# Kernel optimization log

Hardware: AMD Instinct MI355X
Metric: run time of the kernel (lower is better)

The kernel has to match this reference:

```python
import jax, jax.numpy as jnp
import numpy as np

N = 100000      # nodes
E = 1000000     # edges (before self-loops)
IN_DIM = 256
H = 4           # heads
C = 32          # out_dim per head
NEG_SLOPE = 0.2  # PyG GATConv default negative_slope


def setup_inputs() -> dict:
    key = jax.random.key(0)
    ks = jax.random.split(key, 6)
    x = jax.random.normal(ks[0], (N, IN_DIM), jnp.float32)
    W = jax.random.normal(ks[1], (IN_DIM, H * C), jnp.float32) * (1.0 / np.sqrt(IN_DIM))
    a_src = jax.random.normal(ks[2], (H, C), jnp.float32) * 0.1
    a_dst = jax.random.normal(ks[3], (H, C), jnp.float32) * 0.1
    bias = jnp.zeros((H * C,), jnp.float32)
    edge_index = jax.random.randint(ks[4], (2, E), 0, N, dtype=jnp.int32)
    return {"x": x, "W": W, "a_src": a_src, "a_dst": a_dst, "bias": bias,
            "edge_index": edge_index}


def reference(x, W, a_src, a_dst, bias, edge_index):
    n = x.shape[0]
    # PyG GATConv default: add self-loops
    loops = jnp.arange(n, dtype=edge_index.dtype)
    src = jnp.concatenate([edge_index[0], loops])  # [E+N]
    dst = jnp.concatenate([edge_index[1], loops])  # [E+N]
    # linear transform -> [N, H, C]
    h = (x @ W).reshape(n, H, C)
    # per-node attention logits
    alpha_s = jnp.einsum('nhc,hc->nh', h, a_src)  # [N, H]
    alpha_d = jnp.einsum('nhc,hc->nh', h, a_dst)  # [N, H]
    # per-edge score, LeakyReLU
    e = jax.nn.leaky_relu(alpha_s[src] + alpha_d[dst], NEG_SLOPE)  # [E+N, H]
    # segment softmax over incoming edges of each destination node
    m = jax.lax.stop_gradient(jax.ops.segment_max(e, dst, num_segments=n))
    p = jnp.exp(e - m[dst])
    s = jax.ops.segment_sum(p, dst, num_segments=n)
    alpha = p / (s[dst] + 1e-16)  # [E+N, H]
    # weighted scatter-add of source features
    out = jax.ops.segment_sum(alpha[:, :, None] * h[src], dst, num_segments=n)  # [N, H, C]
    out = out.reshape(n, H * C) + bias
    return jnp.tanh(out)
```

## Files before the change

### kernel.cpp

```cpp
#include <hip/hip_runtime.h>

#define IN_DIM 256
#define HC     128
#define NHEAD  4
#define NEG    0.2f
#define BKT    1024
#define NBMAX  128
#define EPT    16
#define BE     4096

typedef __attribute__((ext_vector_type(8))) short short8v;
typedef __attribute__((ext_vector_type(4))) float f32x4;
typedef __attribute__((ext_vector_type(4))) unsigned short ushort4v;

__device__ __forceinline__ unsigned short bf16_rn(float f) {
    unsigned u = __builtin_bit_cast(unsigned, f);
    return (unsigned short)((u + 0x7fffu + ((u >> 16) & 1u)) >> 16);
}
__device__ __forceinline__ float bf16_to_f32(unsigned short b) {
    unsigned u = ((unsigned)b) << 16;
    return __builtin_bit_cast(float, u);
}
__device__ __forceinline__ float bf16_lo(unsigned v) {
    return __builtin_bit_cast(float, v << 16);
}
__device__ __forceinline__ float bf16_hi(unsigned v) {
    return __builtin_bit_cast(float, v & 0xffff0000u);
}
__device__ __forceinline__ float fast_tanh(float x) {
    float t = __expf(2.f * x);
    return fmaf(-2.f, __builtin_amdgcn_rcpf(t + 1.f), 1.f);
}
__device__ __forceinline__ float lrelu(float e) {
    return fmaxf(e, NEG * e);
}

__global__ void pack_w_kernel(const float* __restrict__ W,
                              unsigned short* __restrict__ w_hi) {
    int t = blockIdx.x * 256 + threadIdx.x;
    if (t >= 8 * 8 * 64) return;
    int l  = t & 63;
    int ct = (t >> 6) & 7;
    int s  = t >> 9;
    int kbase = s * 32 + (l >> 4) * 8;
    int col   = ct * 16 + (l & 15);
    size_t base = (size_t)t * 8;
#pragma unroll
    for (int e = 0; e < 8; ++e)
        w_hi[base + e] = bf16_rn(W[(size_t)(kbase + e) * HC + col]);
}

__global__ __launch_bounds__(512) void gemm_mfma_kernel(const float* __restrict__ x,
                                                        const unsigned short* __restrict__ w_hi,
                                                        const float* __restrict__ a_src,
                                                        const float* __restrict__ a_dst,
                                                        unsigned short* __restrict__ h_bf,
                                                        float* __restrict__ alpha_s,
                                                        float* __restrict__ alpha_d, int n) {
    __shared__ unsigned short s_bf[64 * 256];
    __shared__ float pS[64][4];
    __shared__ float pD[64][4];

    const int tid = threadIdx.x;
    const int l   = tid & 63;
    const int wv  = tid >> 6;
    const int row0 = blockIdx.x * 64;

    const float4* x4 = reinterpret_cast<const float4*>(x);
#pragma unroll
    for (int i = 0; i < 8; ++i) {
        int row = i * 8 + wv;
        int c4  = l;
        float4 v = make_float4(0.f, 0.f, 0.f, 0.f);
        if (row0 + row < n) v = x4[(size_t)(row0 + row) * 64 + c4];
        ushort4v b;
        b[0] = bf16_rn(v.x); b[1] = bf16_rn(v.y);
        b[2] = bf16_rn(v.z); b[3] = bf16_rn(v.w);
        int slot = (c4 >> 1) ^ (row & 7);
        int uidx = row * 256 + (slot << 3) + ((c4 & 1) << 2);
        *reinterpret_cast<ushort4v*>(&s_bf[uidx]) = b;
    }
    __syncthreads();

    const int ct_g = wv & 3;
    const int rt_g = wv >> 2;
    const int rrow = l & 15;
    const int kq   = l >> 4;

    f32x4 acc[2][2];
#pragma unroll
    for (int a = 0; a < 2; ++a)
#pragma unroll
        for (int b = 0; b < 2; ++b) acc[a][b] = (f32x4){0.f, 0.f, 0.f, 0.f};

    for (int s = 0; s < 8; ++s) {
        short8v bh[2];
#pragma unroll
        for (int c = 0; c < 2; ++c) {
            int ct = ct_g * 2 + c;
            bh[c] = *reinterpret_cast<const short8v*>(w_hi + ((size_t)(s * 8 + ct) * 64 + l) * 8);
        }
#pragma unroll
        for (int r = 0; r < 2; ++r) {
            int arow = rt_g * 32 + r * 16 + rrow;
            int c16  = kq + s * 4;
            int uidx = arow * 256 + ((c16 ^ (arow & 7)) << 3);
            short8v ah = *reinterpret_cast<const short8v*>(&s_bf[uidx]);
#pragma unroll
            for (int c = 0; c < 2; ++c)
                acc[r][c] = __builtin_amdgcn_mfma_f32_16x16x32_bf16(ah, bh[c], acc[r][c], 0, 0, 0);
        }
    }

#pragma unroll
    for (int r = 0; r < 2; ++r) {
#pragma unroll
        for (int c = 0; c < 2; ++c) {
            int col = (ct_g * 2 + c) * 16 + (l & 15);
#pragma unroll
            for (int q = 0; q < 4; ++q) {
                int row = row0 + rt_g * 32 + r * 16 + (l >> 4) * 4 + q;
                if (row < n) h_bf[(size_t)row * HC + col] = bf16_rn(acc[r][c][q]);
            }
        }
    }

    float asc[2], adc[2];
#pragma unroll
    for (int c = 0; c < 2; ++c) {
        int col = (ct_g * 2 + c) * 16 + (l & 15);
        asc[c] = a_src[col];
        adc[c] = a_dst[col];
    }
#pragma unroll
    for (int r = 0; r < 2; ++r) {
#pragma unroll
        for (int q = 0; q < 4; ++q) {
            float vS = acc[r][0][q] * asc[0] + acc[r][1][q] * asc[1];
            float vD = acc[r][0][q] * adc[0] + acc[r][1][q] * adc[1];
#pragma unroll
            for (int m = 1; m < 16; m <<= 1) {
                vS += __shfl_xor(vS, m);
                vD += __shfl_xor(vD, m);
            }
            if ((l & 15) == 0) {
                int rl = rt_g * 32 + r * 16 + (l >> 4) * 4 + q;
                pS[rl][ct_g] = vS;
                pD[rl][ct_g] = vD;
            }
        }
    }
    __syncthreads();
    if (tid < 256) {
        int rl = tid >> 2, h = tid & 3;
        int row = row0 + rl;
        if (row < n) {
            alpha_s[(size_t)row * 4 + h] = pS[rl][h];
            alpha_d[(size_t)row * 4 + h] = pD[rl][h];
        }
    }
}

__global__ __launch_bounds__(256) void bucket_hist_kernel(const int* __restrict__ ei,
                                                          int* __restrict__ bucket_cnt,
                                                          int E, int nb) {
    __shared__ int lh[NBMAX];
    int tid = threadIdx.x;
    if (tid < NBMAX) lh[tid] = 0;
    __syncthreads();
    int base = blockIdx.x * BE;
#pragma unroll
    for (int i = 0; i < EPT; ++i) {
        int e = base + i * 256 + tid;
        if (e < E) atomicAdd(&lh[ei[E + e] >> 10], 1);
    }
    __syncthreads();
    if (tid < nb && lh[tid]) atomicAdd(&bucket_cnt[tid], lh[tid]);
}

__global__ __launch_bounds__(128) void bucket_scan_kernel(const int* __restrict__ bucket_cnt,
                                                          int* __restrict__ bucket_base,
                                                          int* __restrict__ bucket_cursor,
                                                          int nb) {
    __shared__ int ws0[1];
    int t = threadIdx.x;
    int v = (t < nb) ? bucket_cnt[t] : 0;
    int lane = t & 63, wd = t >> 6;
    int x = v;
#pragma unroll
    for (int off = 1; off < 64; off <<= 1) {
        int y = __shfl_up(x, off);
        if (lane >= off) x += y;
    }
    if (wd == 0 && lane == 63) ws0[0] = x;
    __syncthreads();
    int wo = wd ? ws0[0] : 0;
    int excl = wo + x - v;
    if (t < nb) { bucket_base[t] = excl; bucket_cursor[t] = excl; }
    if (t == 127) bucket_base[nb] = wo + x;
}

__global__ __launch_bounds__(256) void bucket_scatter_kernel(const int* __restrict__ ei,
                                                             int* __restrict__ bucket_cursor,
                                                             unsigned* __restrict__ bucket_data,
                                                             int E, int nb) {
    __shared__ int lh[NBMAX];
    __shared__ int lofs[NBMAX];
    __shared__ int gofs[NBMAX];
    __shared__ int ws0[1];
    __shared__ unsigned buf[BE];

    int tid = threadIdx.x;
    if (tid < NBMAX) lh[tid] = 0;
    __syncthreads();

    int base = blockIdx.x * BE;
    int bb[EPT]; unsigned wv[EPT]; int rr[EPT];
#pragma unroll
    for (int i = 0; i < EPT; ++i) {
        int e = base + i * 256 + tid;
        if (e < E) {
            int src = ei[e];
            int dst = ei[E + e];
            bb[i] = dst >> 10;
            wv[i] = (unsigned)src | ((unsigned)(dst & 1023) << 17);
            rr[i] = atomicAdd(&lh[bb[i]], 1);
        } else bb[i] = -1;
    }
    __syncthreads();

    int v_ = 0, x_ = 0;
    int lane = tid & 63, wd = tid >> 6;
    if (tid < NBMAX) {
        v_ = lh[tid]; x_ = v_;
#pragma unroll
        for (int off = 1; off < 64; off <<= 1) {
            int y = __shfl_up(x_, off);
            if (lane >= off) x_ += y;
        }
        if (wd == 0 && lane == 63) ws0[0] = x_;
    }
    __syncthreads();
    if (tid < NBMAX) {
        int wo = wd ? ws0[0] : 0;
        lofs[tid] = wo + x_ - v_;
    }
    __syncthreads();

#pragma unroll
    for (int i = 0; i < EPT; ++i)
        if (bb[i] >= 0) buf[lofs[bb[i]] + rr[i]] = wv[i];
    if (tid < nb) gofs[tid] = lh[tid] ? atomicAdd(&bucket_cursor[tid], lh[tid]) : 0;
    __syncthreads();

    int wid = tid >> 6;
    for (int bk = wid; bk < nb; bk += 4) {
        int lo = lofs[bk], cnt = lh[bk], g = gofs[bk];
        for (int j = lane; j < cnt; j += 64)
            bucket_data[g + j] = buf[lo + j];
    }
}

__global__ __launch_bounds__(1024) void bucket_build_kernel(const int* __restrict__ bucket_base,
                                                            const unsigned* __restrict__ bucket_data,
                                                            int* __restrict__ deg,
                                                            int* __restrict__ row_start,
                                                            int* __restrict__ csr_src, int n) {
    __shared__ int lc[BKT];
    __shared__ int sc[BKT];
    __shared__ int wsum[16];

    int b = blockIdx.x;
    int base = bucket_base[b];
    int end  = bucket_base[b + 1];
    int t = threadIdx.x;

    lc[t] = 0;
    __syncthreads();
    for (int i = base + t; i < end; i += 1024)
        atomicAdd(&lc[bucket_data[i] >> 17], 1);
    __syncthreads();

    int val = lc[t];
    int lane = t & 63, wd = t >> 6;
    int x = val;
#pragma unroll
    for (int off = 1; off < 64; off <<= 1) {
        int y = __shfl_up(x, off);
        if (lane >= off) x += y;
    }
    if (lane == 63) wsum[wd] = x;
    __syncthreads();
    if (wd == 0 && lane < 16) {
        int y = wsum[lane];
#pragma unroll
        for (int off = 1; off < 16; off <<= 1) {
            int z = __shfl_up(y, off);
            if (lane >= off) y += z;
        }
        wsum[lane] = y;
    }
    __syncthreads();
    int wo = wd ? wsum[wd - 1] : 0;
    int excl = wo + x - val;
    sc[t] = excl;
    int v = b * BKT + t;
    if (v < n) { deg[v] = val; row_start[v] = base + excl; }
    lc[t] = 0;
    __syncthreads();

    for (int i = base + t; i < end; i += 1024) {
        unsigned w = bucket_data[i];
        int d = w >> 17;
        int src = (int)(w & 0x1FFFFu);
        int p = atomicAdd(&lc[d], 1);
        csr_src[base + sc[d] + p] = src;
    }
}

__global__ __launch_bounds__(256) void gather_kernel(const int* __restrict__ row_start,
                                                     const int* __restrict__ deg,
                                                     const int* __restrict__ csr_src,
                                                     const float* __restrict__ alpha_s,
                                                     const float* __restrict__ alpha_d,
                                                     const unsigned short* __restrict__ h_bf,
                                                     const float* __restrict__ bias,
                                                     float* __restrict__ out, int n) {
    int lane = threadIdx.x & 63;
    int wid  = threadIdx.x >> 6;
    int v = blockIdx.x * 4 + wid;
    if (v >= n) return;
    int start = row_start[v];
    int cnt = deg[v];
    int head = lane >> 4;

    const unsigned* hb = reinterpret_cast<const unsigned*>(h_bf);

    float adH = alpha_d[(size_t)v * 4 + head];
    float asH = alpha_s[(size_t)v * 4 + head];
    float pself = __expf(lrelu(asH + adH));
    unsigned hv0 = hb[((unsigned)v << 6) + lane];
    float s = pself;
    float accx = pself * bf16_lo(hv0);
    float accy = pself * bf16_hi(hv0);

    int j = 0;
    for (; j + 8 <= cnt; j += 8) {
        int s0 = csr_src[start + j + 0];
        int s1 = csr_src[start + j + 1];
        int s2 = csr_src[start + j + 2];
        int s3 = csr_src[start + j + 3];
        int s4 = csr_src[start + j + 4];
        int s5 = csr_src[start + j + 5];
        int s6 = csr_src[start + j + 6];
        int s7 = csr_src[start + j + 7];
        float a0 = alpha_s[(size_t)s0 * 4 + head];
        float a1 = alpha_s[(size_t)s1 * 4 + head];
        float a2 = alpha_s[(size_t)s2 * 4 + head];
        float a3 = alpha_s[(size_t)s3 * 4 + head];
        float a4 = alpha_s[(size_t)s4 * 4 + head];
        float a5 = alpha_s[(size_t)s5 * 4 + head];
        float a6 = alpha_s[(size_t)s6 * 4 + head];
        float a7 = alpha_s[(size_t)s7 * 4 + head];
        unsigned h0 = hb[((unsigned)s0 << 6) + lane];
        unsigned h1 = hb[((unsigned)s1 << 6) + lane];
        unsigned h2 = hb[((unsigned)s2 << 6) + lane];
        unsigned h3 = hb[((unsigned)s3 << 6) + lane];
        unsigned h4 = hb[((unsigned)s4 << 6) + lane];
        unsigned h5 = hb[((unsigned)s5 << 6) + lane];
        unsigned h6 = hb[((unsigned)s6 << 6) + lane];
        unsigned h7 = hb[((unsigned)s7 << 6) + lane];
        float w0 = __expf(lrelu(a0 + adH));
        float w1 = __expf(lrelu(a1 + adH));
        float w2 = __expf(lrelu(a2 + adH));
        float w3 = __expf(lrelu(a3 + adH));
        float w4 = __expf(lrelu(a4 + adH));
        float w5 = __expf(lrelu(a5 + adH));
        float w6 = __expf(lrelu(a6 + adH));
        float w7 = __expf(lrelu(a7 + adH));
        s += w0 + w1 + w2 + w3 + w4 + w5 + w6 + w7;
        accx = fmaf(w0, bf16_lo(h0), accx); accy = fmaf(w0, bf16_hi(h0), accy);
        accx = fmaf(w1, bf16_lo(h1), accx); accy = fmaf(w1, bf16_hi(h1), accy);
        accx = fmaf(w2, bf16_lo(h2), accx); accy = fmaf(w2, bf16_hi(h2), accy);
        accx = fmaf(w3, bf16_lo(h3), accx); accy = fmaf(w3, bf16_hi(h3), accy);
        accx = fmaf(w4, bf16_lo(h4), accx); accy = fmaf(w4, bf16_hi(h4), accy);
        accx = fmaf(w5, bf16_lo(h5), accx); accy = fmaf(w5, bf16_hi(h5), accy);
        accx = fmaf(w6, bf16_lo(h6), accx); accy = fmaf(w6, bf16_hi(h6), accy);
        accx = fmaf(w7, bf16_lo(h7), accx); accy = fmaf(w7, bf16_hi(h7), accy);
    }
    for (; j + 4 <= cnt; j += 4) {
        int s0 = csr_src[start + j + 0];
        int s1 = csr_src[start + j + 1];
        int s2 = csr_src[start + j + 2];
        int s3 = csr_src[start + j + 3];
        float a0 = alpha_s[(size_t)s0 * 4 + head];
        float a1 = alpha_s[(size_t)s1 * 4 + head];
        float a2 = alpha_s[(size_t)s2 * 4 + head];
        float a3 = alpha_s[(size_t)s3 * 4 + head];
        unsigned h0 = hb[((unsigned)s0 << 6) + lane];
        unsigned h1 = hb[((unsigned)s1 << 6) + lane];
        unsigned h2 = hb[((unsigned)s2 << 6) + lane];
        unsigned h3 = hb[((unsigned)s3 << 6) + lane];
        float w0 = __expf(lrelu(a0 + adH));
        float w1 = __expf(lrelu(a1 + adH));
        float w2 = __expf(lrelu(a2 + adH));
        float w3 = __expf(lrelu(a3 + adH));
        s += w0 + w1 + w2 + w3;
        accx = fmaf(w0, bf16_lo(h0), accx); accy = fmaf(w0, bf16_hi(h0), accy);
        accx = fmaf(w1, bf16_lo(h1), accx); accy = fmaf(w1, bf16_hi(h1), accy);
        accx = fmaf(w2, bf16_lo(h2), accx); accy = fmaf(w2, bf16_hi(h2), accy);
        accx = fmaf(w3, bf16_lo(h3), accx); accy = fmaf(w3, bf16_hi(h3), accy);
    }
    for (; j < cnt; ++j) {
        int s0 = csr_src[start + j];
        float a0 = alpha_s[(size_t)s0 * 4 + head];
        unsigned h0 = hb[((unsigned)s0 << 6) + lane];
        float w0 = __expf(lrelu(a0 + adH));
        s += w0;
        accx = fmaf(w0, bf16_lo(h0), accx);
        accy = fmaf(w0, bf16_hi(h0), accy);
    }

    float invH = __builtin_amdgcn_rcpf(s + 1e-16f);
    float2 b = reinterpret_cast<const float2*>(bias)[lane];
    float2 o;
    o.x = fast_tanh(fmaf(accx, invH, b.x));
    o.y = fast_tanh(fmaf(accy, invH, b.y));
    reinterpret_cast<float2*>(out)[(size_t)v * 64 + lane] = o;
}

extern "C" void kernel_launch(void* const* d_in, const int* in_sizes, int n_in,
                              void* d_out, int out_size, void* d_ws, size_t ws_size,
                              hipStream_t stream) {
    const float* x     = (const float*)d_in[0];
    const float* W     = (const float*)d_in[1];
    const float* a_src = (const float*)d_in[2];
    const float* a_dst = (const float*)d_in[3];
    const float* bias  = (const float*)d_in[4];
    const int*   ei    = (const int*)d_in[5];

    const int n = in_sizes[0] / IN_DIM;
    const int E = in_sizes[5] / 2;
    const int nb = (n + BKT - 1) / BKT;

    float* ws = (float*)d_ws;
    size_t off = 0;
    unsigned short* h_bf = (unsigned short*)(ws + off); off += (size_t)n * HC / 2;
    float* alpha_s = ws + off; off += (size_t)n * NHEAD;
    float* alpha_d = ws + off; off += (size_t)n * NHEAD;
    unsigned short* w_hi = (unsigned short*)(ws + off); off += 16384;
    int* ibase        = (int*)(ws + off);
    int* deg          = ibase;
    int* row_start    = ibase + n;
    int* bucket_cnt   = ibase + 2 * (size_t)n;
    int* bucket_base  = bucket_cnt + NBMAX;
    int* bucket_cursor= bucket_base + NBMAX + 1;
    unsigned* bucket_data = (unsigned*)(bucket_cursor + NBMAX);
    int* csr_src      = (int*)(bucket_data + E);

    float* out = (float*)d_out;

    const int nblkE = (E + BE - 1) / BE;

    hipMemsetAsync(bucket_cnt, 0, NBMAX * sizeof(int), stream);

    pack_w_kernel<<<16, 256, 0, stream>>>(W, w_hi);
    gemm_mfma_kernel<<<(n + 63) / 64, 512, 0, stream>>>(x, w_hi, a_src, a_dst,
                                                        h_bf, alpha_s, alpha_d, n);

    bucket_hist_kernel<<<nblkE, 256, 0, stream>>>(ei, bucket_cnt, E, nb);
    bucket_scan_kernel<<<1, 128, 0, stream>>>(bucket_cnt, bucket_base, bucket_cursor, nb);
    bucket_scatter_kernel<<<nblkE, 256, 0, stream>>>(ei, bucket_cursor, bucket_data, E, nb);
    bucket_build_kernel<<<nb, 1024, 0, stream>>>(bucket_base, bucket_data,
                                                 deg, row_start, csr_src, n);

    gather_kernel<<<(n + 3) / 4, 256, 0, stream>>>(row_start, deg, csr_src,
                                                   alpha_s, alpha_d, h_bf, bias, out, n);
}
```

Baseline: 146.5 us.

## Merge weight packing into histogram and GEMM into bucket scatter launches

Folds the W packing kernel into the bucket histogram launch as extra blocks, and runs the edge bucket scatter and the node GEMM in one launch, with blocks choosing their role by block index and sharing a union of shared-memory layouts. The scatter path now uses 512 threads with 8 edges per thread instead of 256 with 16. This cuts two kernel launches and lets the compute-bound GEMM blocks overlap with the memory- and atomic-bound scatter blocks. In exchange, the union's shared-memory footprint applies to every block and the scatter blocks use a larger block size, which may change occupancy.

```diff
diff --git a/kernel.cpp b/kernel.cpp
--- a/kernel.cpp
+++ b/kernel.cpp
@@ -6,8 +6,9 @@
 #define NEG    0.2f
 #define BKT    1024
 #define NBMAX  128
-#define EPT    16
+#define EPT2   8
 #define BE     4096
+#define PACKB  16
 
 typedef __attribute__((ext_vector_type(8))) short short8v;
 typedef __attribute__((ext_vector_type(4))) float f32x4;
@@ -17,10 +18,6 @@
     unsigned u = __builtin_bit_cast(unsigned, f);
     return (unsigned short)((u + 0x7fffu + ((u >> 16) & 1u)) >> 16);
 }
-__device__ __forceinline__ float bf16_to_f32(unsigned short b) {
-    unsigned u = ((unsigned)b) << 16;
-    return __builtin_bit_cast(float, u);
-}
 __device__ __forceinline__ float bf16_lo(unsigned v) {
     return __builtin_bit_cast(float, v << 16);
 }
@@ -35,142 +32,31 @@
     return fmaxf(e, NEG * e);
 }
 
-__global__ void pack_w_kernel(const float* __restrict__ W,
-                              unsigned short* __restrict__ w_hi) {
-    int t = blockIdx.x * 256 + threadIdx.x;
-    if (t >= 8 * 8 * 64) return;
-    int l  = t & 63;
-    int ct = (t >> 6) & 7;
-    int s  = t >> 9;
-    int kbase = s * 32 + (l >> 4) * 8;
-    int col   = ct * 16 + (l & 15);
-    size_t base = (size_t)t * 8;
-#pragma unroll
-    for (int e = 0; e < 8; ++e)
-        w_hi[base + e] = bf16_rn(W[(size_t)(kbase + e) * HC + col]);
-}
-
-__global__ __launch_bounds__(512) void gemm_mfma_kernel(const float* __restrict__ x,
-                                                        const unsigned short* __restrict__ w_hi,
-                                                        const float* __restrict__ a_src,
-                                                        const float* __restrict__ a_dst,
-                                                        unsigned short* __restrict__ h_bf,
-                                                        float* __restrict__ alpha_s,
-                                                        float* __restrict__ alpha_d, int n) {
-    __shared__ unsigned short s_bf[64 * 256];
-    __shared__ float pS[64][4];
-    __shared__ float pD[64][4];
-
-    const int tid = threadIdx.x;
-    const int l   = tid & 63;
-    const int wv  = tid >> 6;
-    const int row0 = blockIdx.x * 64;
-
-    const float4* x4 = reinterpret_cast<const float4*>(x);
-#pragma unroll
-    for (int i = 0; i < 8; ++i) {
-        int row = i * 8 + wv;
-        int c4  = l;
-        float4 v = make_float4(0.f, 0.f, 0.f, 0.f);
-        if (row0 + row < n) v = x4[(size_t)(row0 + row) * 64 + c4];
-        ushort4v b;
-        b[0] = bf16_rn(v.x); b[1] = bf16_rn(v.y);
-        b[2] = bf16_rn(v.z); b[3] = bf16_rn(v.w);
-        int slot = (c4 >> 1) ^ (row & 7);
-        int uidx = row * 256 + (slot << 3) + ((c4 & 1) << 2);
-        *reinterpret_cast<ushort4v*>(&s_bf[uidx]) = b;
-    }
-    __syncthreads();
-
-    const int ct_g = wv & 3;
-    const int rt_g = wv >> 2;
-    const int rrow = l & 15;
-    const int kq   = l >> 4;
-
-    f32x4 acc[2][2];
-#pragma unroll
-    for (int a = 0; a < 2; ++a)
-#pragma unroll
-        for (int b = 0; b < 2; ++b) acc[a][b] = (f32x4){0.f, 0.f, 0.f, 0.f};
-
-    for (int s = 0; s < 8; ++s) {
-        short8v bh[2];
-#pragma unroll
-        for (int c = 0; c < 2; ++c) {
-            int ct = ct_g * 2 + c;
-            bh[c] = *reinterpret_cast<const short8v*>(w_hi + ((size_t)(s * 8 + ct) * 64 + l) * 8);
-        }
-#pragma unroll
-        for (int r = 0; r < 2; ++r) {
-            int arow = rt_g * 32 + r * 16 + rrow;
-            int c16  = kq + s * 4;
-            int uidx = arow * 256 + ((c16 ^ (arow & 7)) << 3);
-            short8v ah = *reinterpret_cast<const short8v*>(&s_bf[uidx]);
-#pragma unroll
-            for (int c = 0; c < 2; ++c)
-                acc[r][c] = __builtin_amdgcn_mfma_f32_16x16x32_bf16(ah, bh[c], acc[r][c], 0, 0, 0);
-        }
-    }
-
-#pragma unroll
-    for (int r = 0; r < 2; ++r) {
-#pragma unroll
-        for (int c = 0; c < 2; ++c) {
-            int col = (ct_g * 2 + c) * 16 + (l & 15);
-#pragma unroll
-            for (int q = 0; q < 4; ++q) {
-                int row = row0 + rt_g * 32 + r * 16 + (l >> 4) * 4 + q;
-                if (row < n) h_bf[(size_t)row * HC + col] = bf16_rn(acc[r][c][q]);
-            }
-        }
-    }
-
-    float asc[2], adc[2];
-#pragma unroll
-    for (int c = 0; c < 2; ++c) {
-        int col = (ct_g * 2 + c) * 16 + (l & 15);
-        asc[c] = a_src[col];
-        adc[c] = a_dst[col];
-    }
-#pragma unroll
-    for (int r = 0; r < 2; ++r) {
-#pragma unroll
-        for (int q = 0; q < 4; ++q) {
-            float vS = acc[r][0][q] * asc[0] + acc[r][1][q] * asc[1];
-            float vD = acc[r][0][q] * adc[0] + acc[r][1][q] * adc[1];
-#pragma unroll
-            for (int m = 1; m < 16; m <<= 1) {
-                vS += __shfl_xor(vS, m);
-                vD += __shfl_xor(vD, m);
-            }
-            if ((l & 15) == 0) {
-                int rl = rt_g * 32 + r * 16 + (l >> 4) * 4 + q;
-                pS[rl][ct_g] = vS;
-                pD[rl][ct_g] = vD;
-            }
-        }
-    }
-    __syncthreads();
-    if (tid < 256) {
-        int rl = tid >> 2, h = tid & 3;
-        int row = row0 + rl;
-        if (row < n) {
-            alpha_s[(size_t)row * 4 + h] = pS[rl][h];
-            alpha_d[(size_t)row * 4 + h] = pD[rl][h];
-        }
-    }
-}
-
-__global__ __launch_bounds__(256) void bucket_hist_kernel(const int* __restrict__ ei,
-                                                          int* __restrict__ bucket_cnt,
-                                                          int E, int nb) {
+__global__ __launch_bounds__(256) void pack_hist_kernel(const float* __restrict__ W,
+                                                        unsigned short* __restrict__ w_hi,
+                                                        const int* __restrict__ ei,
+                                                        int* __restrict__ bucket_cnt,
+                                                        int E, int nb) {
     __shared__ int lh[NBMAX];
     int tid = threadIdx.x;
+    if (blockIdx.x < PACKB) {
+        int t = blockIdx.x * 256 + tid;
+        int l  = t & 63;
+        int ct = (t >> 6) & 7;
+        int s  = t >> 9;
+        int kbase = s * 32 + (l >> 4) * 8;
+        int col   = ct * 16 + (l & 15);
+        size_t base = (size_t)t * 8;
+#pragma unroll
+        for (int e = 0; e < 8; ++e)
+            w_hi[base + e] = bf16_rn(W[(size_t)(kbase + e) * HC + col]);
+        return;
+    }
     if (tid < NBMAX) lh[tid] = 0;
     __syncthreads();
-    int base = blockIdx.x * BE;
-#pragma unroll
-    for (int i = 0; i < EPT; ++i) {
+    int base = (blockIdx.x - PACKB) * BE;
+#pragma unroll
+    for (int i = 0; i < 16; ++i) {
         int e = base + i * 256 + tid;
         if (e < E) atomicAdd(&lh[ei[E + e] >> 10], 1);
     }
@@ -200,64 +86,183 @@
     if (t == 127) bucket_base[nb] = wo + x;
 }
 
-__global__ __launch_bounds__(256) void bucket_scatter_kernel(const int* __restrict__ ei,
-                                                             int* __restrict__ bucket_cursor,
-                                                             unsigned* __restrict__ bucket_data,
-                                                             int E, int nb) {
-    __shared__ int lh[NBMAX];
-    __shared__ int lofs[NBMAX];
-    __shared__ int gofs[NBMAX];
-    __shared__ int ws0[1];
-    __shared__ unsigned buf[BE];
-
-    int tid = threadIdx.x;
-    if (tid < NBMAX) lh[tid] = 0;
-    __syncthreads();
-
-    int base = blockIdx.x * BE;
-    int bb[EPT]; unsigned wv[EPT]; int rr[EPT];
-#pragma unroll
-    for (int i = 0; i < EPT; ++i) {
-        int e = base + i * 256 + tid;
-        if (e < E) {
-            int src = ei[e];
-            int dst = ei[E + e];
-            bb[i] = dst >> 10;
-            wv[i] = (unsigned)src | ((unsigned)(dst & 1023) << 17);
-            rr[i] = atomicAdd(&lh[bb[i]], 1);
-        } else bb[i] = -1;
-    }
-    __syncthreads();
-
-    int v_ = 0, x_ = 0;
-    int lane = tid & 63, wd = tid >> 6;
-    if (tid < NBMAX) {
-        v_ = lh[tid]; x_ = v_;
-#pragma unroll
-        for (int off = 1; off < 64; off <<= 1) {
-            int y = __shfl_up(x_, off);
-            if (lane >= off) x_ += y;
-        }
-        if (wd == 0 && lane == 63) ws0[0] = x_;
-    }
-    __syncthreads();
-    if (tid < NBMAX) {
-        int wo = wd ? ws0[0] : 0;
-        lofs[tid] = wo + x_ - v_;
-    }
-    __syncthreads();
-
-#pragma unroll
-    for (int i = 0; i < EPT; ++i)
-        if (bb[i] >= 0) buf[lofs[bb[i]] + rr[i]] = wv[i];
-    if (tid < nb) gofs[tid] = lh[tid] ? atomicAdd(&bucket_cursor[tid], lh[tid]) : 0;
-    __syncthreads();
-
-    int wid = tid >> 6;
-    for (int bk = wid; bk < nb; bk += 4) {
-        int lo = lofs[bk], cnt = lh[bk], g = gofs[bk];
-        for (int j = lane; j < cnt; j += 64)
-            bucket_data[g + j] = buf[lo + j];
+union KSmem {
+    struct {
+        unsigned short s_bf[64 * 256];
+        float pS[64][4];
+        float pD[64][4];
+    } g;
+    struct {
+        int lh[NBMAX];
+        int lofs[NBMAX];
+        int gofs[NBMAX];
+        int ws0;
+        unsigned buf[BE];
+    } s;
+};
+
+__global__ __launch_bounds__(512) void scatter_gemm_kernel(const int* __restrict__ ei,
+                                                           int* __restrict__ bucket_cursor,
+                                                           unsigned* __restrict__ bucket_data,
+                                                           int E, int nb, int nblkE,
+                                                           const float* __restrict__ x,
+                                                           const unsigned short* __restrict__ w_hi,
+                                                           const float* __restrict__ a_src,
+                                                           const float* __restrict__ a_dst,
+                                                           unsigned short* __restrict__ h_bf,
+                                                           float* __restrict__ alpha_s,
+                                                           float* __restrict__ alpha_d, int n) {
+    __shared__ KSmem sm;
+    const int tid = threadIdx.x;
+
+    if ((int)blockIdx.x < nblkE) {
+        if (tid < NBMAX) sm.s.lh[tid] = 0;
+        __syncthreads();
+
+        int base = blockIdx.x * BE;
+        int bb[EPT2]; unsigned wv[EPT2]; int rr[EPT2];
+#pragma unroll
+        for (int i = 0; i < EPT2; ++i) {
+            int e = base + i * 512 + tid;
+            if (e < E) {
+                int src = ei[e];
+                int dst = ei[E + e];
+                bb[i] = dst >> 10;
+                wv[i] = (unsigned)src | ((unsigned)(dst & 1023) << 17);
+                rr[i] = atomicAdd(&sm.s.lh[bb[i]], 1);
+            } else bb[i] = -1;
+        }
+        __syncthreads();
+
+        int lane = tid & 63, wd = tid >> 6;
+        int v_ = 0, x_ = 0;
+        if (tid < NBMAX) {
+            v_ = sm.s.lh[tid]; x_ = v_;
+#pragma unroll
+            for (int off = 1; off < 64; off <<= 1) {
+                int y = __shfl_up(x_, off);
+                if (lane >= off) x_ += y;
+            }
+            if (wd == 0 && lane == 63) sm.s.ws0 = x_;
+        }
+        __syncthreads();
+        if (tid < NBMAX) {
+            int wo = wd ? sm.s.ws0 : 0;
+            sm.s.lofs[tid] = wo + x_ - v_;
+        }
+        __syncthreads();
+
+#pragma unroll
+        for (int i = 0; i < EPT2; ++i)
+            if (bb[i] >= 0) sm.s.buf[sm.s.lofs[bb[i]] + rr[i]] = wv[i];
+        if (tid < nb) sm.s.gofs[tid] = sm.s.lh[tid] ? atomicAdd(&bucket_cursor[tid], sm.s.lh[tid]) : 0;
+        __syncthreads();
+
+        int wid = tid >> 6;
+        for (int bk = wid; bk < nb; bk += 8) {
+            int lo = sm.s.lofs[bk], cnt = sm.s.lh[bk], g = sm.s.gofs[bk];
+            for (int j = lane; j < cnt; j += 64)
+                bucket_data[g + j] = sm.s.buf[lo + j];
+        }
+        return;
+    }
+
+    const int l   = tid & 63;
+    const int wv_ = tid >> 6;
+    const int row0 = ((int)blockIdx.x - nblkE) * 64;
+
+    const float4* x4 = reinterpret_cast<const float4*>(x);
+#pragma unroll
+    for (int i = 0; i < 8; ++i) {
+        int row = i * 8 + wv_;
+        int c4  = l;
+        float4 v = make_float4(0.f, 0.f, 0.f, 0.f);
+        if (row0 + row < n) v = x4[(size_t)(row0 + row) * 64 + c4];
+        ushort4v b;
+        b[0] = bf16_rn(v.x); b[1] = bf16_rn(v.y);
+        b[2] = bf16_rn(v.z); b[3] = bf16_rn(v.w);
+        int slot = (c4 >> 1) ^ (row & 7);
+        int uidx = row * 256 + (slot << 3) + ((c4 & 1) << 2);
+        *reinterpret_cast<ushort4v*>(&sm.g.s_bf[uidx]) = b;
+    }
+    __syncthreads();
+
+    const int ct_g = wv_ & 3;
+    const int rt_g = wv_ >> 2;
+    const int rrow = l & 15;
+    const int kq   = l >> 4;
+
+    f32x4 acc[2][2];
+#pragma unroll
+    for (int a = 0; a < 2; ++a)
+#pragma unroll
+        for (int b = 0; b < 2; ++b) acc[a][b] = (f32x4){0.f, 0.f, 0.f, 0.f};
+
+    for (int s = 0; s < 8; ++s) {
+        short8v bh[2];
+#pragma unroll
+        for (int c = 0; c < 2; ++c) {
+            int ct = ct_g * 2 + c;
+            bh[c] = *reinterpret_cast<const short8v*>(w_hi + ((size_t)(s * 8 + ct) * 64 + l) * 8);
+        }
+#pragma unroll
+        for (int r = 0; r < 2; ++r) {
+            int arow = rt_g * 32 + r * 16 + rrow;
+            int c16  = kq + s * 4;
+            int uidx = arow * 256 + ((c16 ^ (arow & 7)) << 3);
+            short8v ah = *reinterpret_cast<const short8v*>(&sm.g.s_bf[uidx]);
+#pragma unroll
+            for (int c = 0; c < 2; ++c)
+                acc[r][c] = __builtin_amdgcn_mfma_f32_16x16x32_bf16(ah, bh[c], acc[r][c], 0, 0, 0);
+        }
+    }
+
+#pragma unroll
+    for (int r = 0; r < 2; ++r) {
+#pragma unroll
+        for (int c = 0; c < 2; ++c) {
+            int col = (ct_g * 2 + c) * 16 + (l & 15);
+#pragma unroll
+            for (int q = 0; q < 4; ++q) {
+                int row = row0 + rt_g * 32 + r * 16 + (l >> 4) * 4 + q;
+                if (row < n) h_bf[(size_t)row * HC + col] = bf16_rn(acc[r][c][q]);
+            }
+        }
+    }
+
+    float asc[2], adc[2];
+#pragma unroll
+    for (int c = 0; c < 2; ++c) {
+        int col = (ct_g * 2 + c) * 16 + (l & 15);
+        asc[c] = a_src[col];
+        adc[c] = a_dst[col];
+    }
+#pragma unroll
+    for (int r = 0; r < 2; ++r) {
+#pragma unroll
+        for (int q = 0; q < 4; ++q) {
+            float vS = acc[r][0][q] * asc[0] + acc[r][1][q] * asc[1];
+            float vD = acc[r][0][q] * adc[0] + acc[r][1][q] * adc[1];
+#pragma unroll
+            for (int m = 1; m < 16; m <<= 1) {
+                vS += __shfl_xor(vS, m);
+                vD += __shfl_xor(vD, m);
+            }
+            if ((l & 15) == 0) {
+                int rl = rt_g * 32 + r * 16 + (l >> 4) * 4 + q;
+                sm.g.pS[rl][ct_g] = vS;
+                sm.g.pD[rl][ct_g] = vD;
+            }
+        }
+    }
+    __syncthreads();
+    if (tid < 256) {
+        int rl = tid >> 2, h = tid & 3;
+        int row = row0 + rl;
+        if (row < n) {
+            alpha_s[(size_t)row * 4 + h] = sm.g.pS[rl][h];
+            alpha_d[(size_t)row * 4 + h] = sm.g.pD[rl][h];
+        }
     }
 }
 
@@ -461,16 +466,16 @@
     float* out = (float*)d_out;
 
     const int nblkE = (E + BE - 1) / BE;
+    const int gemmB = (n + 63) / 64;
 
     hipMemsetAsync(bucket_cnt, 0, NBMAX * sizeof(int), stream);
 
-    pack_w_kernel<<<16, 256, 0, stream>>>(W, w_hi);
-    gemm_mfma_kernel<<<(n + 63) / 64, 512, 0, stream>>>(x, w_hi, a_src, a_dst,
-                                                        h_bf, alpha_s, alpha_d, n);
-
-    bucket_hist_kernel<<<nblkE, 256, 0, stream>>>(ei, bucket_cnt, E, nb);
+    pack_hist_kernel<<<PACKB + nblkE, 256, 0, stream>>>(W, w_hi, ei, bucket_cnt, E, nb);
     bucket_scan_kernel<<<1, 128, 0, stream>>>(bucket_cnt, bucket_base, bucket_cursor, nb);
-    bucket_scatter_kernel<<<nblkE, 256, 0, stream>>>(ei, bucket_cursor, bucket_data, E, nb);
+    scatter_gemm_kernel<<<nblkE + gemmB, 512, 0, stream>>>(ei, bucket_cursor, bucket_data,
+                                                           E, nb, nblkE,
+                                                           x, w_hi, a_src, a_dst,
+                                                           h_bf, alpha_s, alpha_d, n);
     bucket_build_kernel<<<nb, 1024, 0, stream>>>(bucket_base, bucket_data,
                                                  deg, row_start, csr_src, n);
 
```

Result: faster. 133.7 us (-8.7%).
